# Kernel tuning notes

Hardware: AMD Instinct MI355X
Metric: run time of the kernel (lower is better)

Reference implementation:

```python
import jax, jax.numpy as jnp
import numpy as np


def setup_inputs() -> dict:
    key = jax.random.key(0)
    kK, kQ = jax.random.split(key)
    B, S, D = 8, 2048, 512
    K = jax.random.normal(kK, (B, S, D), dtype=jnp.float32)
    Q = jax.random.normal(kQ, (B, S, D), dtype=jnp.float32)
    return {"K": K, "Q": Q}


def reference(K, Q):
    # K: [B, S_k, D], Q: [B, S_q, D]
    S_q = Q.shape[1]
    S_k = K.shape[1]
    # Causal mask: -inf strictly above the diagonal (k=1), as in np.triu(..., k=1)
    mask = jnp.where(jnp.triu(jnp.ones((S_q, S_k), dtype=bool), k=1), -jnp.inf, 0.0).astype(jnp.float32)
    # NOTE: original scales by sqrt(window_size_keys) (seq len), and adds mask BEFORE scaling.
    logits = (jnp.einsum('bqd,bkd->bqk', Q, K) + mask) / jnp.sqrt(jnp.float32(S_k))
    return jax.nn.softmax(logits, axis=-1)
```

## Files before the change

### kernel.cpp

```cpp
#include <hip/hip_runtime.h>
#include <hip/hip_bf16.h>
#include <math.h>

#define B_SZ 8
#define SEQ 2048
#define DIM 512

typedef __attribute__((ext_vector_type(8))) short bf16x8;
typedef __attribute__((ext_vector_type(8))) unsigned short u16x8;
typedef __attribute__((ext_vector_type(4))) float f32x4;

#define GLOBAL_AS __attribute__((address_space(1)))
#define LDS_AS __attribute__((address_space(3)))

__device__ __forceinline__ unsigned short f2bf(float f) {
    unsigned int u = __builtin_bit_cast(unsigned int, f);
    u += 0x7fffu + ((u >> 16) & 1u);
    return (unsigned short)(u >> 16);
}

__device__ __forceinline__ void load_lds16(const void* g, void* l) {
    __builtin_amdgcn_global_load_lds((const GLOBAL_AS unsigned int*)g,
                                     (LDS_AS unsigned int*)l, 16, 0, 0);
}

__global__ __launch_bounds__(256)
void convert_kernel(const float* __restrict__ src, unsigned short* __restrict__ dst) {
    int i = blockIdx.x * 256 + threadIdx.x;
    const float4* s = (const float4*)src;
    float4 a = s[2 * i];
    float4 b = s[2 * i + 1];
    u16x8 o;
    o[0] = f2bf(a.x); o[1] = f2bf(a.y); o[2] = f2bf(a.z); o[3] = f2bf(a.w);
    o[4] = f2bf(b.x); o[5] = f2bf(b.y); o[6] = f2bf(b.z); o[7] = f2bf(b.w);
    ((u16x8*)dst)[i] = o;
}

#define BM 128
#define BK 32
__global__ __launch_bounds__(256)
void logits_mfma(const unsigned short* __restrict__ Qb, const unsigned short* __restrict__ Kb,
                 float* __restrict__ out) {
    const int tk = blockIdx.x, tq = blockIdx.y, b = blockIdx.z;
    if (tk > tq) return;

    __shared__ __align__(16) unsigned short a_lds[BM * BK];
    __shared__ __align__(16) unsigned short b_lds[BM * BK];

    const int t = threadIdx.x;
    const int wave = t >> 6;
    const int lane = t & 63;
    const int l16 = lane & 15;
    const int quad = lane >> 4;
    const int wm = wave >> 1;
    const int wn = wave & 1;

    const unsigned short* Qrow = Qb + ((size_t)b * SEQ + (size_t)tq * BM) * DIM;
    const unsigned short* Krow = Kb + ((size_t)b * SEQ + (size_t)tk * BM) * DIM;

    const int sr = lane >> 2;
    const int kg = lane & 3;

    f32x4 acc[4][4];
#pragma unroll
    for (int i = 0; i < 4; i++)
#pragma unroll
        for (int j = 0; j < 4; j++) acc[i][j] = (f32x4){0.f, 0.f, 0.f, 0.f};

    for (int k0 = 0; k0 < DIM; k0 += BK) {
#pragma unroll
        for (int j = wave; j < 8; j += 4) {
            int row = j * 16 + sr;
            load_lds16(Qrow + (size_t)row * DIM + k0 + kg * 8, &a_lds[(j * 16) * BK]);
            load_lds16(Krow + (size_t)row * DIM + k0 + kg * 8, &b_lds[(j * 16) * BK]);
        }
        __syncthreads();

        bf16x8 af[4], bf[4];
#pragma unroll
        for (int mi = 0; mi < 4; mi++)
            af[mi] = *(const bf16x8*)&a_lds[(wm * 64 + mi * 16 + l16) * BK + quad * 8];
#pragma unroll
        for (int ni = 0; ni < 4; ni++)
            bf[ni] = *(const bf16x8*)&b_lds[(wn * 64 + ni * 16 + l16) * BK + quad * 8];
#pragma unroll
        for (int mi = 0; mi < 4; mi++)
#pragma unroll
            for (int ni = 0; ni < 4; ni++)
                acc[mi][ni] = __builtin_amdgcn_mfma_f32_16x16x32_bf16(af[mi], bf[ni], acc[mi][ni], 0, 0, 0);
        __syncthreads();
    }

    const float scale = 0.02209708691207961f;
    float* outb = out + (size_t)b * SEQ * SEQ;
#pragma unroll
    for (int mi = 0; mi < 4; mi++) {
#pragma unroll
        for (int ni = 0; ni < 4; ni++) {
            int col = tk * BM + wn * 64 + ni * 16 + l16;
#pragma unroll
            for (int r = 0; r < 4; r++) {
                int row = tq * BM + wm * 64 + mi * 16 + quad * 4 + r;
                outb[(size_t)row * SEQ + col] = acc[mi][ni][r] * scale;
            }
        }
    }
}

__global__ __launch_bounds__(256)
void softmax_kernel(float* __restrict__ out) {
    const int q = blockIdx.x & (SEQ - 1);
    const int b = blockIdx.x >> 11;
    float* row = out + ((size_t)b * SEQ + q) * SEQ;
    const int t = threadIdx.x;
    const int lane = t & 63;
    const int wave = t >> 6;
    const int n = q + 1;

    __shared__ float red[8];

    float4 v[2];
    float m = -INFINITY;
#pragma unroll
    for (int j = 0; j < 2; j++) {
        int k0 = (t + j * 256) * 4;
        if (k0 < n) {
            float4 x = *(const float4*)(row + k0);
            x.y = (k0 + 1 < n) ? x.y : -INFINITY;
            x.z = (k0 + 2 < n) ? x.z : -INFINITY;
            x.w = (k0 + 3 < n) ? x.w : -INFINITY;
            v[j] = x;
            m = fmaxf(m, fmaxf(fmaxf(x.x, x.y), fmaxf(x.z, x.w)));
        } else {
            v[j] = (float4){-INFINITY, -INFINITY, -INFINITY, -INFINITY};
        }
    }
#pragma unroll
    for (int off = 1; off < 64; off <<= 1) m = fmaxf(m, __shfl_xor(m, off));
    if (lane == 0) red[wave] = m;
    __syncthreads();
    m = fmaxf(fmaxf(red[0], red[1]), fmaxf(red[2], red[3]));

    float s = 0.f;
#pragma unroll
    for (int j = 0; j < 2; j++) {
        float4 e;
        e.x = __expf(v[j].x - m);
        e.y = __expf(v[j].y - m);
        e.z = __expf(v[j].z - m);
        e.w = __expf(v[j].w - m);
        v[j] = e;
        s += e.x + e.y + e.z + e.w;
    }
#pragma unroll
    for (int off = 1; off < 64; off <<= 1) s += __shfl_xor(s, off);
    if (lane == 0) red[4 + wave] = s;
    __syncthreads();
    s = red[4] + red[5] + red[6] + red[7];
    const float inv = 1.0f / s;

#pragma unroll
    for (int j = 0; j < 2; j++) {
        int k0 = (t + j * 256) * 4;
        float4 e = v[j];
        e.x *= inv; e.y *= inv; e.z *= inv; e.w *= inv;
        *(float4*)(row + k0) = e;
    }
}

#define TS 64
#define DC 128
#define LSTRIDE (DC + 8)
__global__ __launch_bounds__(256)
void logits_fallback(const float* __restrict__ Q, const float* __restrict__ K,
                     float* __restrict__ out) {
    const int tk = blockIdx.x, tq = blockIdx.y, b = blockIdx.z;
    if (tk > tq) return;
    __shared__ __align__(16) unsigned short qs[TS * LSTRIDE];
    __shared__ __align__(16) unsigned short ks[TS * LSTRIDE];
    const int t = threadIdx.x;
    const int wave = t >> 6, lane = t & 63, l16 = lane & 15, quad = lane >> 4;
    const float* Qb = Q + ((size_t)b * SEQ + (size_t)tq * TS) * DIM;
    const float* Kb = K + ((size_t)b * SEQ + (size_t)tk * TS) * DIM;
    f32x4 acc[4];
#pragma unroll
    for (int i = 0; i < 4; i++) acc[i] = (f32x4){0.f, 0.f, 0.f, 0.f};
    for (int c = 0; c < DIM; c += DC) {
        __syncthreads();
#pragma unroll
        for (int i = 0; i < 8; i++) {
            int idx = t + i * 256;
            int row = idx >> 5, c4 = idx & 31;
            float4 qv = *(const float4*)(Qb + row * DIM + c + c4 * 4);
            float4 kv = *(const float4*)(Kb + row * DIM + c + c4 * 4);
            ushort4 qh = { f2bf(qv.x), f2bf(qv.y), f2bf(qv.z), f2bf(qv.w) };
            ushort4 kh = { f2bf(kv.x), f2bf(kv.y), f2bf(kv.z), f2bf(kv.w) };
            *(ushort4*)&qs[row * LSTRIDE + c4 * 4] = qh;
            *(ushort4*)&ks[row * LSTRIDE + c4 * 4] = kh;
        }
        __syncthreads();
#pragma unroll
        for (int d = 0; d < DC; d += 32) {
            bf16x8 afrag = *(const bf16x8*)&qs[(wave * 16 + l16) * LSTRIDE + d + quad * 8];
#pragma unroll
            for (int nt = 0; nt < 4; nt++) {
                bf16x8 bfrag = *(const bf16x8*)&ks[(nt * 16 + l16) * LSTRIDE + d + quad * 8];
                acc[nt] = __builtin_amdgcn_mfma_f32_16x16x32_bf16(afrag, bfrag, acc[nt], 0, 0, 0);
            }
        }
    }
    const float scale = 0.02209708691207961f;
    float* outb = out + (size_t)b * SEQ * SEQ;
#pragma unroll
    for (int nt = 0; nt < 4; nt++) {
        int col = tk * TS + nt * 16 + l16;
#pragma unroll
        for (int r = 0; r < 4; r++) {
            int row = tq * TS + wave * 16 + quad * 4 + r;
            outb[(size_t)row * SEQ + col] = acc[nt][r] * scale;
        }
    }
}

extern "C" void kernel_launch(void* const* d_in, const int* in_sizes, int n_in,
                              void* d_out, int out_size, void* d_ws, size_t ws_size,
                              hipStream_t stream) {
    const float* Kp = (const float*)d_in[0];
    const float* Qp = (const float*)d_in[1];
    float* out = (float*)d_out;

    const size_t nElem = (size_t)B_SZ * SEQ * DIM;
    if (ws_size >= 2 * nElem * sizeof(unsigned short)) {
        unsigned short* Qbf = (unsigned short*)d_ws;
        unsigned short* Kbf = Qbf + nElem;
        int cblocks = (int)(nElem / 8 / 256);
        convert_kernel<<<dim3(cblocks), dim3(256), 0, stream>>>(Qp, Qbf);
        convert_kernel<<<dim3(cblocks), dim3(256), 0, stream>>>(Kp, Kbf);
        logits_mfma<<<dim3(SEQ / BM, SEQ / BM, B_SZ), dim3(256), 0, stream>>>(Qbf, Kbf, out);
    } else {
        logits_fallback<<<dim3(SEQ / TS, SEQ / TS, B_SZ), dim3(256), 0, stream>>>(Qp, Kp, out);
    }
    softmax_kernel<<<dim3(B_SZ * SEQ), dim3(256), 0, stream>>>(out);
}
```

Baseline: 244.2 us.

## Fuse exp into logits epilogue and replace softmax with partial-sum rescale

The logits kernel now applies exp directly (no max subtraction), zeros masked upper-triangle tiles, and writes per-row partial sums to workspace. A light rescale kernel sums the partials and normalizes only the causal part of each row. The two convert launches are merged into one. Skipping the max subtraction risks overflow for large logits, and the workspace-size fallback is removed.

```diff
diff --git a/kernel.cpp b/kernel.cpp
--- a/kernel.cpp
+++ b/kernel.cpp
@@ -25,7 +25,10 @@
 }
 
 __global__ __launch_bounds__(256)
-void convert_kernel(const float* __restrict__ src, unsigned short* __restrict__ dst) {
+void convert_kernel(const float* __restrict__ Qs, const float* __restrict__ Ks,
+                    unsigned short* __restrict__ Qd, unsigned short* __restrict__ Kd) {
+    const float* src = blockIdx.y ? Qs : Ks;
+    unsigned short* dst = blockIdx.y ? Qd : Kd;
     int i = blockIdx.x * 256 + threadIdx.x;
     const float4* s = (const float4*)src;
     float4 a = s[2 * i];
@@ -39,15 +42,26 @@
 #define BM 128
 #define BK 32
 __global__ __launch_bounds__(256)
-void logits_mfma(const unsigned short* __restrict__ Qb, const unsigned short* __restrict__ Kb,
-                 float* __restrict__ out) {
+void logits_exp(const unsigned short* __restrict__ Qb, const unsigned short* __restrict__ Kb,
+                float* __restrict__ out, float* __restrict__ partials) {
     const int tk = blockIdx.x, tq = blockIdx.y, b = blockIdx.z;
-    if (tk > tq) return;
+    const int t = threadIdx.x;
+    float* outb = out + (size_t)b * SEQ * SEQ;
+
+    if (tk > tq) {
+        float4 z = {0.f, 0.f, 0.f, 0.f};
+        float4* o = (float4*)(outb + (size_t)(tq * BM) * SEQ + tk * BM);
+        const int c4 = t & 31;
+        const int r0 = t >> 5;
+#pragma unroll
+        for (int r = 0; r < BM; r += 8)
+            o[(size_t)(r + r0) * (SEQ / 4) + c4] = z;
+        return;
+    }
 
     __shared__ __align__(16) unsigned short a_lds[BM * BK];
     __shared__ __align__(16) unsigned short b_lds[BM * BK];
 
-    const int t = threadIdx.x;
     const int wave = t >> 6;
     const int lane = t & 63;
     const int l16 = lane & 15;
@@ -92,133 +106,56 @@
     }
 
     const float scale = 0.02209708691207961f;
-    float* outb = out + (size_t)b * SEQ * SEQ;
+    const bool diag = (tk == tq);
 #pragma unroll
     for (int mi = 0; mi < 4; mi++) {
+        const int rowb = tq * BM + wm * 64 + mi * 16 + quad * 4;
 #pragma unroll
-        for (int ni = 0; ni < 4; ni++) {
-            int col = tk * BM + wn * 64 + ni * 16 + l16;
+        for (int r = 0; r < 4; r++) {
+            const int row = rowb + r;
+            float psum = 0.f;
 #pragma unroll
-            for (int r = 0; r < 4; r++) {
-                int row = tq * BM + wm * 64 + mi * 16 + quad * 4 + r;
-                outb[(size_t)row * SEQ + col] = acc[mi][ni][r] * scale;
+            for (int ni = 0; ni < 4; ni++) {
+                const int col = tk * BM + wn * 64 + ni * 16 + l16;
+                float e = __expf(acc[mi][ni][r] * scale);
+                e = (!diag || col <= row) ? e : 0.f;
+                psum += e;
+                outb[(size_t)row * SEQ + col] = e;
             }
+            psum += __shfl_xor(psum, 1);
+            psum += __shfl_xor(psum, 2);
+            psum += __shfl_xor(psum, 4);
+            psum += __shfl_xor(psum, 8);
+            if (l16 == 0)
+                partials[((size_t)b * SEQ + row) * 32 + tk * 2 + wn] = psum;
         }
     }
 }
 
 __global__ __launch_bounds__(256)
-void softmax_kernel(float* __restrict__ out) {
+void rescale_kernel(float* __restrict__ out, const float* __restrict__ partials) {
     const int q = blockIdx.x & (SEQ - 1);
     const int b = blockIdx.x >> 11;
-    float* row = out + ((size_t)b * SEQ + q) * SEQ;
     const int t = threadIdx.x;
     const int lane = t & 63;
-    const int wave = t >> 6;
-    const int n = q + 1;
+    const int tqt = q >> 7;
+    const int nslots = (tqt + 1) * 2;
 
-    __shared__ float red[8];
+    float v = 0.f;
+    if (lane < nslots) v = partials[((size_t)(b * SEQ + q)) * 32 + lane];
+    v += __shfl_xor(v, 1);
+    v += __shfl_xor(v, 2);
+    v += __shfl_xor(v, 4);
+    v += __shfl_xor(v, 8);
+    v += __shfl_xor(v, 16);
+    const float inv = 1.0f / __shfl(v, 0);
 
-    float4 v[2];
-    float m = -INFINITY;
-#pragma unroll
-    for (int j = 0; j < 2; j++) {
-        int k0 = (t + j * 256) * 4;
-        if (k0 < n) {
-            float4 x = *(const float4*)(row + k0);
-            x.y = (k0 + 1 < n) ? x.y : -INFINITY;
-            x.z = (k0 + 2 < n) ? x.z : -INFINITY;
-            x.w = (k0 + 3 < n) ? x.w : -INFINITY;
-            v[j] = x;
-            m = fmaxf(m, fmaxf(fmaxf(x.x, x.y), fmaxf(x.z, x.w)));
-        } else {
-            v[j] = (float4){-INFINITY, -INFINITY, -INFINITY, -INFINITY};
-        }
-    }
-#pragma unroll
-    for (int off = 1; off < 64; off <<= 1) m = fmaxf(m, __shfl_xor(m, off));
-    if (lane == 0) red[wave] = m;
-    __syncthreads();
-    m = fmaxf(fmaxf(red[0], red[1]), fmaxf(red[2], red[3]));
-
-    float s = 0.f;
-#pragma unroll
-    for (int j = 0; j < 2; j++) {
-        float4 e;
-        e.x = __expf(v[j].x - m);
-        e.y = __expf(v[j].y - m);
-        e.z = __expf(v[j].z - m);
-        e.w = __expf(v[j].w - m);
-        v[j] = e;
-        s += e.x + e.y + e.z + e.w;
-    }
-#pragma unroll
-    for (int off = 1; off < 64; off <<= 1) s += __shfl_xor(s, off);
-    if (lane == 0) red[4 + wave] = s;
-    __syncthreads();
-    s = red[4] + red[5] + red[6] + red[7];
-    const float inv = 1.0f / s;
-
-#pragma unroll
-    for (int j = 0; j < 2; j++) {
-        int k0 = (t + j * 256) * 4;
-        float4 e = v[j];
+    float4* row = (float4*)(out + ((size_t)b * SEQ + q) * SEQ);
+    const int n4 = (tqt + 1) * 32;
+    for (int i = t; i < n4; i += 256) {
+        float4 e = row[i];
         e.x *= inv; e.y *= inv; e.z *= inv; e.w *= inv;
-        *(float4*)(row + k0) = e;
-    }
-}
-
-#define TS 64
-#define DC 128
-#define LSTRIDE (DC + 8)
-__global__ __launch_bounds__(256)
-void logits_fallback(const float* __restrict__ Q, const float* __restrict__ K,
-                     float* __restrict__ out) {
-    const int tk = blockIdx.x, tq = blockIdx.y, b = blockIdx.z;
-    if (tk > tq) return;
-    __shared__ __align__(16) unsigned short qs[TS * LSTRIDE];
-    __shared__ __align__(16) unsigned short ks[TS * LSTRIDE];
-    const int t = threadIdx.x;
-    const int wave = t >> 6, lane = t & 63, l16 = lane & 15, quad = lane >> 4;
-    const float* Qb = Q + ((size_t)b * SEQ + (size_t)tq * TS) * DIM;
-    const float* Kb = K + ((size_t)b * SEQ + (size_t)tk * TS) * DIM;
-    f32x4 acc[4];
-#pragma unroll
-    for (int i = 0; i < 4; i++) acc[i] = (f32x4){0.f, 0.f, 0.f, 0.f};
-    for (int c = 0; c < DIM; c += DC) {
-        __syncthreads();
-#pragma unroll
-        for (int i = 0; i < 8; i++) {
-            int idx = t + i * 256;
-            int row = idx >> 5, c4 = idx & 31;
-            float4 qv = *(const float4*)(Qb + row * DIM + c + c4 * 4);
-            float4 kv = *(const float4*)(Kb + row * DIM + c + c4 * 4);
-            ushort4 qh = { f2bf(qv.x), f2bf(qv.y), f2bf(qv.z), f2bf(qv.w) };
-            ushort4 kh = { f2bf(kv.x), f2bf(kv.y), f2bf(kv.z), f2bf(kv.w) };
-            *(ushort4*)&qs[row * LSTRIDE + c4 * 4] = qh;
-            *(ushort4*)&ks[row * LSTRIDE + c4 * 4] = kh;
-        }
-        __syncthreads();
-#pragma unroll
-        for (int d = 0; d < DC; d += 32) {
-            bf16x8 afrag = *(const bf16x8*)&qs[(wave * 16 + l16) * LSTRIDE + d + quad * 8];
-#pragma unroll
-            for (int nt = 0; nt < 4; nt++) {
-                bf16x8 bfrag = *(const bf16x8*)&ks[(nt * 16 + l16) * LSTRIDE + d + quad * 8];
-                acc[nt] = __builtin_amdgcn_mfma_f32_16x16x32_bf16(afrag, bfrag, acc[nt], 0, 0, 0);
-            }
-        }
-    }
-    const float scale = 0.02209708691207961f;
-    float* outb = out + (size_t)b * SEQ * SEQ;
-#pragma unroll
-    for (int nt = 0; nt < 4; nt++) {
-        int col = tk * TS + nt * 16 + l16;
-#pragma unroll
-        for (int r = 0; r < 4; r++) {
-            int row = tq * TS + wave * 16 + quad * 4 + r;
-            outb[(size_t)row * SEQ + col] = acc[nt][r] * scale;
-        }
+        row[i] = e;
     }
 }
 
@@ -230,15 +167,11 @@
     float* out = (float*)d_out;
 
     const size_t nElem = (size_t)B_SZ * SEQ * DIM;
-    if (ws_size >= 2 * nElem * sizeof(unsigned short)) {
-        unsigned short* Qbf = (unsigned short*)d_ws;
-        unsigned short* Kbf = Qbf + nElem;
-        int cblocks = (int)(nElem / 8 / 256);
-        convert_kernel<<<dim3(cblocks), dim3(256), 0, stream>>>(Qp, Qbf);
-        convert_kernel<<<dim3(cblocks), dim3(256), 0, stream>>>(Kp, Kbf);
-        logits_mfma<<<dim3(SEQ / BM, SEQ / BM, B_SZ), dim3(256), 0, stream>>>(Qbf, Kbf, out);
-    } else {
-        logits_fallback<<<dim3(SEQ / TS, SEQ / TS, B_SZ), dim3(256), 0, stream>>>(Qp, Kp, out);
-    }
-    softmax_kernel<<<dim3(B_SZ * SEQ), dim3(256), 0, stream>>>(out);
+    unsigned short* Qbf = (unsigned short*)d_ws;
+    unsigned short* Kbf = Qbf + nElem;
+    float* partials = (float*)(Kbf + nElem);
+
+    convert_kernel<<<dim3((unsigned)(nElem / 2048), 2), dim3(256), 0, stream>>>(Qp, Kp, Qbf, Kbf);
+    logits_exp<<<dim3(SEQ / BM, SEQ / BM, B_SZ), dim3(256), 0, stream>>>(Qbf, Kbf, out, partials);
+    rescale_kernel<<<dim3(B_SZ * SEQ), dim3(256), 0, stream>>>(out, partials);
 }
```

After: 253.2 us. 1.04x slower.
